# Kernel tuning notes

Measured on AMD Instinct MI355X. Metric: run time of the kernel, lower is better.

## Reference

```python
import jax, jax.numpy as jnp
import numpy as np

B, L, H, Di, N, K, R = 2, 512, 2048, 4096, 16, 4, 128


def setup_inputs() -> dict:
    key = jax.random.key(0)
    ks = jax.random.split(key, 8)
    s = 0.02
    inp = {
        "x": jax.random.normal(ks[0], (B, L, H), jnp.float32),
        "in_w": jax.random.normal(ks[1], (2 * Di, H), jnp.float32) * s,
        "in_b": jnp.zeros((2 * Di,), jnp.float32),
        "conv_w": jax.random.normal(ks[2], (Di, 1, K), jnp.float32) * s,  # depthwise conv weight
        "conv_b": jnp.zeros((Di,), jnp.float32),
        "xproj_w": jax.random.normal(ks[3], (R + 2 * N, Di), jnp.float32) * s,
        "dt_w": jax.random.normal(ks[4], (Di, R), jnp.float32) * s,
        "dt_b": jax.random.normal(ks[5], (Di,), jnp.float32) * 0.1,
        "A_log": jnp.log(jnp.broadcast_to(jnp.arange(1, N + 1, dtype=jnp.float32)[None, :], (Di, N))) + jnp.zeros((Di, N), jnp.float32),
        "D": jnp.ones((Di,), jnp.float32),
        "out_w": jax.random.normal(ks[6], (H, Di), jnp.float32) * s,
        "out_b": jnp.zeros((H,), jnp.float32),
    }
    return inp


def reference(x, in_w, in_b, conv_w, conv_b, xproj_w, dt_w, dt_b, A_log, D, out_w, out_b):
    silu = jax.nn.silu
    # in_proj -> split into hidden path and gate
    proj = x @ in_w.T + in_b                       # [B, L, 2*Di]
    h, gate = jnp.split(proj, 2, axis=-1)          # each [B, L, Di]
    # causal depthwise conv1d over time
    hc = jnp.transpose(h, (0, 2, 1))               # [B, Di, L]
    hc = jax.lax.conv_general_dilated(
        hc, conv_w, window_strides=(1,), padding=[(K - 1, 0)],
        dimension_numbers=("NCH", "OIH", "NCH"), feature_group_count=Di)
    hc = silu(hc + conv_b[None, :, None])          # [B, Di, L]
    hs = jnp.transpose(hc, (0, 2, 1))              # [B, L, Di]
    # input-dependent SSM parameters
    sp = hs @ xproj_w.T                            # [B, L, R + 2N]
    ts, Bm, Cm = sp[..., :R], sp[..., R:R + N], sp[..., R + N:]
    dt = jax.nn.softplus(ts @ dt_w.T + dt_b)       # [B, L, Di]
    A = -jnp.exp(A_log)                            # [Di, N]
    dA = jnp.exp(dt[..., None] * A[None, None])    # [B, L, Di, N]
    dBu = dt[..., None] * Bm[:, :, None, :] * hs[..., None]  # [B, L, Di, N]

    # selective scan: s_t = dA_t * s_{t-1} + dBu_t ; y_t = s_t . C_t
    def step(s, inputs):
        dA_t, dBu_t, C_t = inputs                  # [B,Di,N], [B,Di,N], [B,N]
        s = dA_t * s + dBu_t
        y = jnp.einsum("bdn,bn->bd", s, C_t)
        return s, y

    s0 = jnp.zeros((x.shape[0], Di, N), x.dtype)
    _, ys = jax.lax.scan(step, s0, (jnp.swapaxes(dA, 0, 1), jnp.swapaxes(dBu, 0, 1), jnp.swapaxes(Cm, 0, 1)))
    y = jnp.transpose(ys, (1, 0, 2))               # [B, L, Di]
    y = (y + hs * D) * silu(gate)
    return y @ out_w.T + out_b                     # [B, L, H]
```

## Files before the change

### kernel.cpp

```cpp
#include <hip/hip_runtime.h>
#include <hip/hip_bf16.h>

typedef __hip_bfloat16 bf16;
typedef _Float16 fp16;
typedef short bf16x8 __attribute__((ext_vector_type(8)));
typedef float f32x4 __attribute__((ext_vector_type(4)));
typedef _Float16 half8 __attribute__((ext_vector_type(8)));
typedef _Float16 half2v __attribute__((ext_vector_type(2)));

#define BB 2
#define LL 512
#define HH 2048
#define DI 4096
#define NST 16
#define KK 4
#define RR 128
#define BLM (BB*LL)
#define CN 16
#define LC (LL/CN)
#define ZXP 16
#define ZOUT 4
#define CONV_N (BLM*DI)
#define CONV8_N (CONV_N/8)
#define CVT4_N (HH*DI/4)

enum { MODE_PROJ = 0, MODE_XPROJ = 1, MODE_DT = 2, MODE_OUT = 3 };

__device__ __forceinline__ float sigmoidf_(float x) { return 1.f / (1.f + __expf(-x)); }
__device__ __forceinline__ float softplusf_(float x) {
    return fmaxf(x, 0.f) + log1pf(__expf(-fabsf(x)));
}
__device__ __forceinline__ unsigned int bfpack(float a, float b) {
    __hip_bfloat162 h = __float22bfloat162_rn(make_float2(a, b));
    union { __hip_bfloat162 h; unsigned int u; } cv; cv.h = h;
    return cv.u;
}
__device__ __forceinline__ float b2f(short s) {
    union { unsigned u; float f; } c; c.u = ((unsigned)(unsigned short)s) << 16; return c.f;
}

typedef const __attribute__((address_space(1))) unsigned int* gas_t;
typedef __attribute__((address_space(3))) unsigned int* las_t;
__device__ __forceinline__ void gld16(const void* g, void* l) {
    __builtin_amdgcn_global_load_lds((gas_t)g, (las_t)l, 16, 0, 0);
}

__device__ __forceinline__ void cvt_seg(const float* s, bf16* d, int i) {
    float4 v = ((const float4*)s)[i];
    uint2 o; o.x = bfpack(v.x, v.y); o.y = bfpack(v.z, v.w);
    ((uint2*)d)[i] = o;
}

__global__ __launch_bounds__(256) void cvt_all(
    const float* __restrict__ s0, bf16* __restrict__ d0, int n0,
    const float* __restrict__ s1, bf16* __restrict__ d1, int n1,
    const float* __restrict__ s2, bf16* __restrict__ d2, int n2,
    const float* __restrict__ s3, bf16* __restrict__ d3, int n3)
{
    int i = blockIdx.x * 256 + threadIdx.x;
    int stride = gridDim.x * 256;
    int t1 = n0 + n1, t2 = t1 + n2, t3 = t2 + n3;
    for (; i < t3; i += stride) {
        if      (i < n0) cvt_seg(s0, d0, i);
        else if (i < t1) cvt_seg(s1, d1, i - n0);
        else if (i < t2) cvt_seg(s2, d2, i - t1);
        else             cvt_seg(s3, d3, i - t2);
    }
}

template<int BM, int BN, int MODE>
__global__ __launch_bounds__(256) void gemm_bf16(
    const bf16* __restrict__ A, const bf16* __restrict__ Bw,
    int N, int K, int lda, int ldb,
    const float* __restrict__ bias,
    bf16* __restrict__ outh, bf16* __restrict__ outh2,
    fp16* __restrict__ s0, fp16* __restrict__ s1,
    fp16* __restrict__ s2, fp16* __restrict__ s3)
{
    __shared__ short sA[BM * 64];
    __shared__ short sB[BN * 64];
    const int tid = threadIdx.x;
    const int col0 = blockIdx.x * BN;
    const int row0 = blockIdx.y * BM;
    const int wave = tid >> 6;
    const int lane = tid & 63;
    constexpr int NJR = (BM == 64 || BN == 64) ? 2 : 4;
    const int wr = (BM == 128) ? ((wave >> 1) * 64) : 0;
    const int wc = (BM == 64) ? (wave * 32) : ((wave & 1) * (BN / 2));
    const int lr = lane & 15;
    const int q  = lane >> 4;
    const int sw = lane & 7;

    const int kpb = K / gridDim.z;
    const int kbeg = blockIdx.z * kpb;
    const int kend = kbeg + kpb;

    const int r0 = tid >> 3;
    const int kc  = (tid & 7) << 3;
    const int kcs = (((tid & 7) ^ ((tid >> 3) & 7)) << 3);

    f32x4 acc[4][NJR] = {};

    for (int k0 = kbeg; k0 < kend; k0 += 64) {
        #pragma unroll
        for (int p = 0; p < BM / 32; p++) {
            int r = r0 + p * 32;
            gld16(A + (size_t)(row0 + r) * lda + k0 + kcs, &sA[r * 64 + kc]);
        }
        #pragma unroll
        for (int p = 0; p < BN / 32; p++) {
            int rr = r0 + p * 32;
            int nb = col0 + rr; if (nb > N - 1) nb = N - 1;
            gld16(Bw + (size_t)nb * ldb + k0 + kcs, &sB[rr * 64 + kc]);
        }
        __syncthreads();
        bf16x8 af[2][4], bfr[2][NJR];
        #pragma unroll
        for (int kk = 0; kk < 2; kk++) {
            const int cs = ((kk * 4 + q) ^ sw) << 3;
            #pragma unroll
            for (int i = 0; i < 4; i++)
                af[kk][i] = *(const bf16x8*)(&sA[(wr + i * 16 + lr) * 64 + cs]);
            #pragma unroll
            for (int j = 0; j < NJR; j++)
                bfr[kk][j] = *(const bf16x8*)(&sB[(wc + j * 16 + lr) * 64 + cs]);
        }
        #pragma unroll
        for (int kk = 0; kk < 2; kk++)
            #pragma unroll
            for (int i = 0; i < 4; i++)
                #pragma unroll
                for (int j = 0; j < NJR; j++)
                    acc[i][j] = __builtin_amdgcn_mfma_f32_16x16x32_bf16(af[kk][i], bfr[kk][j], acc[i][j], 0, 0, 0);
        __syncthreads();
    }

    fp16* oslice = s0;
    if (MODE == MODE_OUT) {
        int z = blockIdx.z;
        oslice = (z == 0) ? s0 : (z == 1) ? s1 : (z == 2) ? s2 : s3;
    }
    const int drow = (lane >> 4) << 2;
    const int dcol = lane & 15;
    #pragma unroll
    for (int i = 0; i < 4; i++) {
        #pragma unroll
        for (int j = 0; j < NJR; j++) {
            int n = col0 + wc + j * 16 + dcol;
            if (n >= N) continue;
            float bv = bias ? bias[n] : 0.f;
            #pragma unroll
            for (int r = 0; r < 4; r++) {
                int m = row0 + wr + i * 16 + drow + r;
                float v = acc[i][j][r];
                if (MODE == MODE_PROJ) {
                    v += bv;
                    if (n < DI) outh2[(size_t)m * DI + n] = (bf16)v;
                    else        outh[(size_t)m * DI + (n - DI)] = (bf16)v;
                } else if (MODE == MODE_XPROJ) {
                    s0[(size_t)blockIdx.z * (BLM * 160) + (size_t)m * 160 + n] = (fp16)v;
                } else if (MODE == MODE_DT) {
                    s0[(size_t)m * DI + n] = (fp16)softplusf_(v + bv);
                } else {
                    oslice[(size_t)m * HH + n] = (fp16)v;
                }
            }
        }
    }
}

__global__ __launch_bounds__(256) void conv_cvtow(
    const bf16* __restrict__ h, const float* __restrict__ conv_w,
    const float* __restrict__ conv_b, bf16* __restrict__ hs_b,
    const float* __restrict__ ow, bf16* __restrict__ ow_b)
{
    int i = blockIdx.x * 256 + threadIdx.x;
    int stride = gridDim.x * 256;
    for (; i < CONV8_N + CVT4_N; i += stride) {
        if (i < CONV8_N) {
            int idx = i << 3;
            int d0 = idx & (DI - 1);
            int l = (idx >> 12) & (LL - 1);
            float4 cb0 = *(const float4*)&conv_b[d0];
            float4 cb1 = *(const float4*)&conv_b[d0 + 4];
            float acc[8] = {cb0.x, cb0.y, cb0.z, cb0.w, cb1.x, cb1.y, cb1.z, cb1.w};
            float4 w[8];
            #pragma unroll
            for (int j = 0; j < 8; j++) w[j] = *(const float4*)&conv_w[(d0 + j) * KK];
            #pragma unroll
            for (int k = 0; k < KK; k++) {
                int ls = l - (KK - 1) + k;
                if (ls >= 0) {
                    bf16x8 hv = *(const bf16x8*)&h[(size_t)idx + (size_t)(ls - l) * DI];
                    #pragma unroll
                    for (int j = 0; j < 8; j++)
                        acc[j] += b2f(hv[j]) * ((const float*)&w[j])[k];
                }
            }
            uint4 o;
            float s0 = acc[0] * sigmoidf_(acc[0]), s1 = acc[1] * sigmoidf_(acc[1]);
            float s2 = acc[2] * sigmoidf_(acc[2]), s3 = acc[3] * sigmoidf_(acc[3]);
            float s4 = acc[4] * sigmoidf_(acc[4]), s5 = acc[5] * sigmoidf_(acc[5]);
            float s6 = acc[6] * sigmoidf_(acc[6]), s7 = acc[7] * sigmoidf_(acc[7]);
            o.x = bfpack(s0, s1); o.y = bfpack(s2, s3);
            o.z = bfpack(s4, s5); o.w = bfpack(s6, s7);
            *(uint4*)&hs_b[idx] = o;
        } else {
            cvt_seg(ow, ow_b, i - CONV8_N);
        }
    }
}

__global__ __launch_bounds__(256) void reduce_sp(
    const fp16* __restrict__ spS, float* __restrict__ sp_f, bf16* __restrict__ ts_b)
{
    int i = blockIdx.x * 256 + threadIdx.x;
    int row = i / 80, c2 = (i % 80) * 2;
    float r0 = 0.f, r1 = 0.f;
    #pragma unroll
    for (int z = 0; z < ZXP; z++) {
        half2v v = *(const half2v*)&spS[(size_t)z * (BLM * 160) + (size_t)row * 160 + c2];
        r0 += (float)v[0]; r1 += (float)v[1];
    }
    *(float2*)&sp_f[(size_t)row * 160 + c2] = make_float2(r0, r1);
    if (c2 < RR) *(unsigned*)&ts_b[(size_t)row * RR + c2] = bfpack(r0, r1);
}

__global__ __launch_bounds__(256) void reduce_out(
    const fp16* __restrict__ s0, const fp16* __restrict__ s1,
    const fp16* __restrict__ s2, const fp16* __restrict__ s3,
    const float* __restrict__ bias, float* __restrict__ out)
{
    int i = blockIdx.x * 256 + threadIdx.x;
    int c8 = (i & 255) << 3;
    half8 a = ((const half8*)s0)[i];
    half8 b = ((const half8*)s1)[i];
    half8 c = ((const half8*)s2)[i];
    half8 d = ((const half8*)s3)[i];
    float r[8];
    #pragma unroll
    for (int e = 0; e < 8; e++)
        r[e] = (float)a[e] + (float)b[e] + (float)c[e] + (float)d[e] + bias[c8 + e];
    ((float4*)out)[2 * i]     = make_float4(r[0], r[1], r[2], r[3]);
    ((float4*)out)[2 * i + 1] = make_float4(r[4], r[5], r[6], r[7]);
}

__global__ __launch_bounds__(256) void scan_part1(
    const fp16* __restrict__ dtr, const float* __restrict__ sp,
    const bf16* __restrict__ hs_b, const float* __restrict__ A_log,
    float* __restrict__ P_ws, float* __restrict__ S_ws)
{
    int bid = blockIdx.x;
    int c  = bid & (CN - 1);
    int db = (bid >> 4) & 63;
    int b  = bid >> 10;
    int ng = threadIdx.x >> 6;
    int d  = db * 64 + (threadIdx.x & 63);
    int n0 = ng * 4;

    float A[4], P[4], S[4];
    #pragma unroll
    for (int k = 0; k < 4; k++) {
        A[k] = -__expf(A_log[d * NST + n0 + k]);
        P[k] = 1.f; S[k] = 0.f;
    }
    const float* spb = sp + (size_t)b * LL * 160;
    size_t base = (size_t)b * LL * DI + d;
    for (int l = c * LC; l < (c + 1) * LC; l++) {
        size_t off = base + (size_t)l * DI;
        float dtv = (float)dtr[off];
        float hsv = (float)hs_b[off];
        float dh = dtv * hsv;
        #pragma unroll
        for (int k = 0; k < 4; k++) {
            float a  = __expf(dtv * A[k]);
            float Bn = spb[l * 160 + RR + n0 + k];
            S[k] = a * S[k] + dh * Bn;
            P[k] *= a;
        }
    }
    size_t ob = (size_t)(b * CN + c) * NST * DI + (size_t)n0 * DI + d;
    #pragma unroll
    for (int k = 0; k < 4; k++) {
        P_ws[ob + (size_t)k * DI] = P[k];
        S_ws[ob + (size_t)k * DI] = S[k];
    }
}

__global__ __launch_bounds__(256) void scan_mid(
    const float* __restrict__ P_ws, float* __restrict__ S_ws)
{
    int bid = blockIdx.x;
    int n  = bid & (NST - 1);
    int db = (bid >> 4) & (DI / 256 - 1);
    int b  = bid >> 8;
    int d  = db * 256 + threadIdx.x;
    size_t base = (size_t)n * DI + d;
    float s = 0.f;
    for (int c = 0; c < CN; c++) {
        size_t idx = (size_t)(b * CN + c) * NST * DI + base;
        float p  = P_ws[idx];
        float sv = S_ws[idx];
        S_ws[idx] = s;
        s = p * s + sv;
    }
}

__global__ __launch_bounds__(256) void scan_part2(
    const fp16* __restrict__ dtr, const float* __restrict__ sp,
    const bf16* __restrict__ hs_b, const bf16* __restrict__ g_b,
    const float* __restrict__ A_log, const float* __restrict__ Dv,
    const float* __restrict__ I_ws, bf16* __restrict__ y_b)
{
    int bid = blockIdx.x;
    int c  = bid & (CN - 1);
    int db = (bid >> 4) & 63;
    int b  = bid >> 10;
    int ng = threadIdx.x & 3;
    int d  = db * 64 + (threadIdx.x >> 2);
    int n0 = ng * 4;

    float A[4], s[4];
    #pragma unroll
    for (int k = 0; k < 4; k++)
        A[k] = -__expf(A_log[d * NST + n0 + k]);
    size_t ib = (size_t)(b * CN + c) * NST * DI + (size_t)n0 * DI + d;
    #pragma unroll
    for (int k = 0; k < 4; k++) s[k] = I_ws[ib + (size_t)k * DI];
    float Dd = Dv[d];

    const float* spb = sp + (size_t)b * LL * 160;
    size_t base = (size_t)b * LL * DI + d;
    for (int l = c * LC; l < (c + 1) * LC; l++) {
        size_t off = base + (size_t)l * DI;
        float dtv = (float)dtr[off];
        float hsv = (float)hs_b[off];
        float dh = dtv * hsv;
        float y = 0.f;
        #pragma unroll
        for (int k = 0; k < 4; k++) {
            float a  = __expf(dtv * A[k]);
            float Bn = spb[l * 160 + RR + n0 + k];
            float Cn = spb[l * 160 + RR + NST + n0 + k];
            s[k] = a * s[k] + dh * Bn;
            y += s[k] * Cn;
        }
        y += __shfl_xor(y, 1);
        y += __shfl_xor(y, 2);
        if (ng == 0) {
            float gv = (float)g_b[off];
            y_b[off] = (bf16)((y + hsv * Dd) * (gv * sigmoidf_(gv)));
        }
    }
}

extern "C" void kernel_launch(void* const* d_in, const int* in_sizes, int n_in,
                              void* d_out, int out_size, void* d_ws, size_t ws_size,
                              hipStream_t stream)
{
    const float* x       = (const float*)d_in[0];
    const float* in_w    = (const float*)d_in[1];
    const float* in_b    = (const float*)d_in[2];
    const float* conv_w  = (const float*)d_in[3];
    const float* conv_b  = (const float*)d_in[4];
    const float* xproj_w = (const float*)d_in[5];
    const float* dt_w    = (const float*)d_in[6];
    const float* dt_b    = (const float*)d_in[7];
    const float* A_log   = (const float*)d_in[8];
    const float* Dv      = (const float*)d_in[9];
    const float* out_w   = (const float*)d_in[10];
    const float* out_b   = (const float*)d_in[11];
    float* out = (float*)d_out;

    char* ws = (char*)d_ws;
    const size_t MB = 1u << 20;
    bf16*  h_b    = (bf16*)(ws);
    fp16*  spS    = (fp16*)(ws);
    float* P_ws   = (float*)(ws);
    fp16*  oS0    = (fp16*)(ws);
    fp16*  oS1    = (fp16*)(ws + 4 * MB);
    bf16*  x_b    = (bf16*)(ws + 8 * MB);
    float* S_ws   = (float*)(ws + 8 * MB);
    fp16*  oS2    = (fp16*)(ws + 8 * MB);
    fp16*  oS3    = (fp16*)(ws + 12 * MB);
    bf16*  in_w_b = (bf16*)(ws + 16 * MB);
    bf16*  ow_b   = (bf16*)(ws + 16 * MB);
    bf16*  y_b    = (bf16*)(ws + 32 * MB);
    fp16*  dt_h   = (fp16*)(ws + 40 * MB);
    bf16*  hs_b   = (bf16*)(ws + 48 * MB);
    bf16*  g_b    = (bf16*)(ws + 56 * MB);
    char* p = ws + 64 * MB;
    float* sp_f = (float*)p; p += (size_t)BLM * 160 * 4;
    bf16*  ts_b = (bf16*)p;  p += (size_t)BLM * RR * 2;
    bf16*  xw_b = (bf16*)p;  p += (size_t)(RR + 2 * NST) * DI * 2;
    bf16*  dtw_b= (bf16*)p;  p += (size_t)DI * RR * 2;

    cvt_all<<<2048, 256, 0, stream>>>(
        x, x_b, BLM * HH / 4,
        in_w, in_w_b, 2 * DI * HH / 4,
        xproj_w, xw_b, (RR + 2 * NST) * DI / 4,
        dt_w, dtw_b, DI * RR / 4);
    gemm_bf16<128, 64, MODE_PROJ><<<dim3((2 * DI) / 64, BLM / 128, 1), 256, 0, stream>>>(
        x_b, in_w_b, 2 * DI, HH, HH, HH, in_b, g_b, h_b,
        nullptr, nullptr, nullptr, nullptr);
    conv_cvtow<<<2048, 256, 0, stream>>>(h_b, conv_w, conv_b, hs_b, out_w, ow_b);
    gemm_bf16<64, 128, MODE_XPROJ><<<dim3(2, BLM / 64, ZXP), 256, 0, stream>>>(
        hs_b, xw_b, RR + 2 * NST, DI, DI, DI, nullptr, nullptr, nullptr,
        spS, nullptr, nullptr, nullptr);
    reduce_sp<<<320, 256, 0, stream>>>(spS, sp_f, ts_b);
    gemm_bf16<64, 128, MODE_DT><<<dim3(DI / 128, BLM / 64, 1), 256, 0, stream>>>(
        ts_b, dtw_b, DI, RR, RR, RR, dt_b, nullptr, nullptr,
        dt_h, nullptr, nullptr, nullptr);
    scan_part1<<<BB * (DI / 64) * CN, 256, 0, stream>>>(
        dt_h, sp_f, hs_b, A_log, P_ws, S_ws);
    scan_mid<<<BB * NST * (DI / 256), 256, 0, stream>>>(P_ws, S_ws);
    scan_part2<<<BB * (DI / 64) * CN, 256, 0, stream>>>(
        dt_h, sp_f, hs_b, g_b, A_log, Dv, S_ws, y_b);
    gemm_bf16<128, 128, MODE_OUT><<<dim3(HH / 128, BLM / 128, ZOUT), 256, 0, stream>>>(
        y_b, ow_b, HH, DI, DI, DI, nullptr, nullptr, nullptr,
        oS0, oS1, oS2, oS3);
    reduce_out<<<1024, 256, 0, stream>>>(oS0, oS1, oS2, oS3, out_b, out);
}
```

Measured before the change: 346.1 us.

## Fuse split-K output reduction via atomics and fold scan_mid into scan_part2

The output GEMM's split-K partials are now accumulated directly into the fp32 output with atomicAdd, after the conv kernel pre-fills the output with the bias. This removes the fp16 partial buffers and the separate reduce_out launch. The chunk-carry pass scan_mid is removed: each scan_part2 block recomputes its incoming state by serially combining the earlier chunks' P/S values. That saves a launch but adds redundant work that grows with chunk index. Atomics make the result order nondeterministic and add contention among the four K-slices.

After: 382.5 us. 1.11x slower.

```diff
diff --git a/kernel.cpp b/kernel.cpp
--- a/kernel.cpp
+++ b/kernel.cpp
@@ -23,6 +23,7 @@
 #define CONV_N (BLM*DI)
 #define CONV8_N (CONV_N/8)
 #define CVT4_N (HH*DI/4)
+#define OUTB4_N (BLM*HH/4)
 
 enum { MODE_PROJ = 0, MODE_XPROJ = 1, MODE_DT = 2, MODE_OUT = 3 };
 
@@ -74,8 +75,7 @@
     int N, int K, int lda, int ldb,
     const float* __restrict__ bias,
     bf16* __restrict__ outh, bf16* __restrict__ outh2,
-    fp16* __restrict__ s0, fp16* __restrict__ s1,
-    fp16* __restrict__ s2, fp16* __restrict__ s3)
+    fp16* __restrict__ s0, float* __restrict__ outf)
 {
     __shared__ short sA[BM * 64];
     __shared__ short sB[BN * 64];
@@ -135,11 +135,6 @@
         __syncthreads();
     }
 
-    fp16* oslice = s0;
-    if (MODE == MODE_OUT) {
-        int z = blockIdx.z;
-        oslice = (z == 0) ? s0 : (z == 1) ? s1 : (z == 2) ? s2 : s3;
-    }
     const int drow = (lane >> 4) << 2;
     const int dcol = lane & 15;
     #pragma unroll
@@ -162,7 +157,7 @@
                 } else if (MODE == MODE_DT) {
                     s0[(size_t)m * DI + n] = (fp16)softplusf_(v + bv);
                 } else {
-                    oslice[(size_t)m * HH + n] = (fp16)v;
+                    atomicAdd(&outf[(size_t)m * HH + n], v);
                 }
             }
         }
@@ -172,11 +167,13 @@
 __global__ __launch_bounds__(256) void conv_cvtow(
     const bf16* __restrict__ h, const float* __restrict__ conv_w,
     const float* __restrict__ conv_b, bf16* __restrict__ hs_b,
-    const float* __restrict__ ow, bf16* __restrict__ ow_b)
+    const float* __restrict__ ow, bf16* __restrict__ ow_b,
+    const float* __restrict__ out_b, float* __restrict__ outf)
 {
     int i = blockIdx.x * 256 + threadIdx.x;
     int stride = gridDim.x * 256;
-    for (; i < CONV8_N + CVT4_N; i += stride) {
+    int t1 = CONV8_N + CVT4_N, t2 = t1 + OUTB4_N;
+    for (; i < t2; i += stride) {
         if (i < CONV8_N) {
             int idx = i << 3;
             int d0 = idx & (DI - 1);
@@ -205,8 +202,12 @@
             o.x = bfpack(s0, s1); o.y = bfpack(s2, s3);
             o.z = bfpack(s4, s5); o.w = bfpack(s6, s7);
             *(uint4*)&hs_b[idx] = o;
+        } else if (i < t1) {
+            cvt_seg(ow, ow_b, i - CONV8_N);
         } else {
-            cvt_seg(ow, ow_b, i - CONV8_N);
+            int j = i - t1;
+            int n4 = j & (HH / 4 - 1);
+            ((float4*)outf)[j] = ((const float4*)out_b)[n4];
         }
     }
 }
@@ -224,25 +225,6 @@
     }
     *(float2*)&sp_f[(size_t)row * 160 + c2] = make_float2(r0, r1);
     if (c2 < RR) *(unsigned*)&ts_b[(size_t)row * RR + c2] = bfpack(r0, r1);
-}
-
-__global__ __launch_bounds__(256) void reduce_out(
-    const fp16* __restrict__ s0, const fp16* __restrict__ s1,
-    const fp16* __restrict__ s2, const fp16* __restrict__ s3,
-    const float* __restrict__ bias, float* __restrict__ out)
-{
-    int i = blockIdx.x * 256 + threadIdx.x;
-    int c8 = (i & 255) << 3;
-    half8 a = ((const half8*)s0)[i];
-    half8 b = ((const half8*)s1)[i];
-    half8 c = ((const half8*)s2)[i];
-    half8 d = ((const half8*)s3)[i];
-    float r[8];
-    #pragma unroll
-    for (int e = 0; e < 8; e++)
-        r[e] = (float)a[e] + (float)b[e] + (float)c[e] + (float)d[e] + bias[c8 + e];
-    ((float4*)out)[2 * i]     = make_float4(r[0], r[1], r[2], r[3]);
-    ((float4*)out)[2 * i + 1] = make_float4(r[4], r[5], r[6], r[7]);
 }
 
 __global__ __launch_bounds__(256) void scan_part1(
@@ -287,30 +269,12 @@
     }
 }
 
-__global__ __launch_bounds__(256) void scan_mid(
-    const float* __restrict__ P_ws, float* __restrict__ S_ws)
-{
-    int bid = blockIdx.x;
-    int n  = bid & (NST - 1);
-    int db = (bid >> 4) & (DI / 256 - 1);
-    int b  = bid >> 8;
-    int d  = db * 256 + threadIdx.x;
-    size_t base = (size_t)n * DI + d;
-    float s = 0.f;
-    for (int c = 0; c < CN; c++) {
-        size_t idx = (size_t)(b * CN + c) * NST * DI + base;
-        float p  = P_ws[idx];
-        float sv = S_ws[idx];
-        S_ws[idx] = s;
-        s = p * s + sv;
-    }
-}
-
 __global__ __launch_bounds__(256) void scan_part2(
     const fp16* __restrict__ dtr, const float* __restrict__ sp,
     const bf16* __restrict__ hs_b, const bf16* __restrict__ g_b,
     const float* __restrict__ A_log, const float* __restrict__ Dv,
-    const float* __restrict__ I_ws, bf16* __restrict__ y_b)
+    const float* __restrict__ P_ws, const float* __restrict__ S_ws,
+    bf16* __restrict__ y_b)
 {
     int bid = blockIdx.x;
     int c  = bid & (CN - 1);
@@ -322,11 +286,16 @@
 
     float A[4], s[4];
     #pragma unroll
-    for (int k = 0; k < 4; k++)
+    for (int k = 0; k < 4; k++) {
         A[k] = -__expf(A_log[d * NST + n0 + k]);
-    size_t ib = (size_t)(b * CN + c) * NST * DI + (size_t)n0 * DI + d;
-    #pragma unroll
-    for (int k = 0; k < 4; k++) s[k] = I_ws[ib + (size_t)k * DI];
+        s[k] = 0.f;
+    }
+    for (int j = 0; j < c; j++) {
+        size_t ojb = (size_t)(b * CN + j) * NST * DI + (size_t)n0 * DI + d;
+        #pragma unroll
+        for (int k = 0; k < 4; k++)
+            s[k] = P_ws[ojb + (size_t)k * DI] * s[k] + S_ws[ojb + (size_t)k * DI];
+    }
     float Dd = Dv[d];
 
     const float* spb = sp + (size_t)b * LL * 160;
@@ -377,12 +346,8 @@
     bf16*  h_b    = (bf16*)(ws);
     fp16*  spS    = (fp16*)(ws);
     float* P_ws   = (float*)(ws);
-    fp16*  oS0    = (fp16*)(ws);
-    fp16*  oS1    = (fp16*)(ws + 4 * MB);
     bf16*  x_b    = (bf16*)(ws + 8 * MB);
     float* S_ws   = (float*)(ws + 8 * MB);
-    fp16*  oS2    = (fp16*)(ws + 8 * MB);
-    fp16*  oS3    = (fp16*)(ws + 12 * MB);
     bf16*  in_w_b = (bf16*)(ws + 16 * MB);
     bf16*  ow_b   = (bf16*)(ws + 16 * MB);
     bf16*  y_b    = (bf16*)(ws + 32 * MB);
@@ -402,22 +367,21 @@
         dt_w, dtw_b, DI * RR / 4);
     gemm_bf16<128, 64, MODE_PROJ><<<dim3((2 * DI) / 64, BLM / 128, 1), 256, 0, stream>>>(
         x_b, in_w_b, 2 * DI, HH, HH, HH, in_b, g_b, h_b,
-        nullptr, nullptr, nullptr, nullptr);
-    conv_cvtow<<<2048, 256, 0, stream>>>(h_b, conv_w, conv_b, hs_b, out_w, ow_b);
+        nullptr, nullptr);
+    conv_cvtow<<<2048, 256, 0, stream>>>(h_b, conv_w, conv_b, hs_b, out_w, ow_b,
+                                         out_b, out);
     gemm_bf16<64, 128, MODE_XPROJ><<<dim3(2, BLM / 64, ZXP), 256, 0, stream>>>(
         hs_b, xw_b, RR + 2 * NST, DI, DI, DI, nullptr, nullptr, nullptr,
-        spS, nullptr, nullptr, nullptr);
+        spS, nullptr);
     reduce_sp<<<320, 256, 0, stream>>>(spS, sp_f, ts_b);
     gemm_bf16<64, 128, MODE_DT><<<dim3(DI / 128, BLM / 64, 1), 256, 0, stream>>>(
         ts_b, dtw_b, DI, RR, RR, RR, dt_b, nullptr, nullptr,
-        dt_h, nullptr, nullptr, nullptr);
+        dt_h, nullptr);
     scan_part1<<<BB * (DI / 64) * CN, 256, 0, stream>>>(
         dt_h, sp_f, hs_b, A_log, P_ws, S_ws);
-    scan_mid<<<BB * NST * (DI / 256), 256, 0, stream>>>(P_ws, S_ws);
     scan_part2<<<BB * (DI / 64) * CN, 256, 0, stream>>>(
-        dt_h, sp_f, hs_b, g_b, A_log, Dv, S_ws, y_b);
+        dt_h, sp_f, hs_b, g_b, A_log, Dv, P_ws, S_ws, y_b);
     gemm_bf16<128, 128, MODE_OUT><<<dim3(HH / 128, BLM / 128, ZOUT), 256, 0, stream>>>(
         y_b, ow_b, HH, DI, DI, DI, nullptr, nullptr, nullptr,
-        oS0, oS1, oS2, oS3);
-    reduce_out<<<1024, 256, 0, stream>>>(oS0, oS1, oS2, oS3, out_b, out);
-}
+        nullptr, out);
+}
```
